# Kernel tuning notes

Measured on AMD Instinct MI355X. Metric: run time of the kernel, lower is better.

## Reference

```python
import jax, jax.numpy as jnp
import numpy as np

N_NODES = 100000
N_EDGES = 1600000
IN_DIM = 64
HID = 64
EDGE_DIM = 1
NUM_GRAPHS = 1000
SCALE = 0.05


def setup_inputs() -> dict:
    key = jax.random.key(0)
    ks = jax.random.split(key, 20)
    x = jax.random.normal(ks[0], (N_NODES, IN_DIM), dtype=jnp.float32)
    edge_index = jax.random.randint(ks[1], (2, N_EDGES), 0, N_NODES, dtype=jnp.int64)
    edge_attr = jax.random.normal(ks[2], (N_EDGES, EDGE_DIM), dtype=jnp.float32)
    batch = jnp.sort(jax.random.randint(ks[3], (N_NODES,), 0, NUM_GRAPHS, dtype=jnp.int64))
    p = lambda k, shp: SCALE * jax.random.normal(k, shp, dtype=jnp.float32)
    return {
        "x": x, "edge_index": edge_index, "edge_attr": edge_attr, "batch": batch,
        # conv1 MLP + edge lin
        "W1a": p(ks[4], (IN_DIM, HID)), "b1a": p(ks[5], (HID,)),
        "W1b": p(ks[6], (HID, HID)), "b1b": p(ks[7], (HID,)),
        "We1": p(ks[8], (EDGE_DIM, IN_DIM)), "be1": p(ks[9], (IN_DIM,)),
        # conv2 MLP + edge lin
        "W2a": p(ks[10], (HID, HID)), "b2a": p(ks[11], (HID,)),
        "W2b": p(ks[12], (HID, HID)), "b2b": p(ks[13], (HID,)),
        "We2": p(ks[14], (EDGE_DIM, HID)), "be2": p(ks[15], (HID,)),
        # classifier
        "Wc1": p(ks[16], (HID, HID)), "bc1": p(ks[17], (HID,)),
        "Wc2": p(ks[18], (HID, 1)), "bc2": p(ks[19], (1,)),
    }


def _gine(x, src, dst, e_proj, Wa, ba, Wb, bb):
    # message: ReLU(x_src + projected edge feature); scatter-sum to target
    msg = jax.nn.relu(x[src] + e_proj)                      # [E, D]
    agg = jax.ops.segment_sum(msg, dst, num_segments=x.shape[0])
    h = x + agg                                             # eps = 0 (default)
    return jax.nn.relu(h @ Wa + ba) @ Wb + bb               # GIN MLP


def reference(x, edge_index, edge_attr, batch,
              W1a, b1a, W1b, b1b, We1, be1,
              W2a, b2a, W2b, b2b, We2, be2,
              Wc1, bc1, Wc2, bc2):
    src, dst = edge_index[0], edge_index[1]
    h = _gine(x, src, dst, edge_attr @ We1 + be1, W1a, b1a, W1b, b1b)
    h = jax.nn.relu(h)  # dropout is identity in eval mode
    h = _gine(h, src, dst, edge_attr @ We2 + be2, W2a, b2a, W2b, b2b)
    h = jax.nn.relu(h)
    # global mean pool over graphs
    sums = jax.ops.segment_sum(h, batch, num_segments=NUM_GRAPHS)
    cnts = jax.ops.segment_sum(jnp.ones((h.shape[0], 1), h.dtype), batch, num_segments=NUM_GRAPHS)
    pooled = sums / jnp.maximum(cnts, 1.0)                  # [G, HID]
    return jax.nn.relu(pooled @ Wc1 + bc1) @ Wc2 + bc2      # [G, 1]
```

## Files before the change

### kernel.cpp

```cpp
#include <hip/hip_runtime.h>

#define N_NODES    100000
#define N_EDGES    1600000
#define DIM        64
#define NUM_GRAPHS 1000
#define CONV_BLK   3125
#define PAD        72

#define SLICES     512
#define SLICE_E    3125
#define NBUCK      782
#define CAP4       3072

typedef __attribute__((ext_vector_type(8))) short bf16x8;
typedef __attribute__((ext_vector_type(4))) float f32x4;

__device__ __forceinline__ unsigned short f2bf(float f) {
    unsigned int b = __float_as_uint(f);
    b += 0x7FFFu + ((b >> 16) & 1u);
    return (unsigned short)(b >> 16);
}

__device__ __forceinline__ float4 ntload_f4(const float* p) {
    f32x4 v = __builtin_nontemporal_load((const f32x4*)p);
    return make_float4(v.x, v.y, v.z, v.w);
}

__global__ __launch_bounds__(256) void prep(
    const int* __restrict__ ei, const float* __restrict__ x,
    int* __restrict__ hist, int* __restrict__ bucketTotal,
    unsigned short* __restrict__ x16)
{
    __shared__ int lh[NBUCK];
    int blk = blockIdx.x, t = threadIdx.x;
    if (blk < SLICES) {
        for (int i = t; i < NBUCK; i += 256) lh[i] = 0;
        __syncthreads();
        const int* dsts = ei + N_EDGES + blk * SLICE_E;
        for (int k = t; k < SLICE_E; k += 256)
            atomicAdd(&lh[dsts[k] >> 7], 1);
        __syncthreads();
        for (int i = t; i < NBUCK; i += 256) {
            int h = lh[i];
            hist[blk * NBUCK + i] = h;
            if (h) atomicAdd(&bucketTotal[i], h);
        }
    } else {
        int tt = (blk - SLICES) * 256 + t;
        if (tt < N_NODES * DIM / 8) {
            int base = tt * 8;
            float4 f0 = ntload_f4(x + base);
            float4 f1 = ntload_f4(x + base + 4);
            uint4 o;
            o.x = (unsigned)f2bf(f0.x) | ((unsigned)f2bf(f0.y) << 16);
            o.y = (unsigned)f2bf(f0.z) | ((unsigned)f2bf(f0.w) << 16);
            o.z = (unsigned)f2bf(f1.x) | ((unsigned)f2bf(f1.y) << 16);
            o.w = (unsigned)f2bf(f1.z) | ((unsigned)f2bf(f1.w) << 16);
            *(uint4*)(x16 + base) = o;
        }
    }
}

__global__ __launch_bounds__(1024) void csr_c2a(
    const int* __restrict__ bucketTotal, int* __restrict__ bucketStart)
{
    __shared__ int sc[1024];
    int t = threadIdx.x;
    int v = (t < NBUCK) ? bucketTotal[t] : 0;
    sc[t] = v;
    __syncthreads();
    for (int o = 1; o < 1024; o <<= 1) {
        int u = (t >= o) ? sc[t - o] : 0;
        __syncthreads();
        sc[t] += u;
        __syncthreads();
    }
    if (t < NBUCK) bucketStart[t] = sc[t] - v;
    if (t == NBUCK - 1) bucketStart[NBUCK] = sc[t];
}

__global__ __launch_bounds__(512) void csr_c2b(
    const int* __restrict__ hist, const int* __restrict__ bucketStart,
    int* __restrict__ off)
{
    __shared__ int sc[512];
    int b = blockIdx.x, t = threadIdx.x;
    int v = hist[t * NBUCK + b];
    sc[t] = v;
    __syncthreads();
    for (int o = 1; o < 512; o <<= 1) {
        int u = (t >= o) ? sc[t - o] : 0;
        __syncthreads();
        sc[t] += u;
        __syncthreads();
    }
    off[b * SLICES + t] = bucketStart[b] + sc[t] - v;
}

__global__ __launch_bounds__(256) void csr_c3(
    const int* __restrict__ ei, const float* __restrict__ ea,
    const int* __restrict__ hist, const int* __restrict__ off,
    int2* __restrict__ tmp)
{
    __shared__ int2 staging[SLICE_E];
    __shared__ int  lstart[NBUCK + 1];
    __shared__ int  garr[NBUCK];
    __shared__ int  lcur[NBUCK];
    __shared__ unsigned short barr[SLICE_E];
    __shared__ int  part[256];

    int s = blockIdx.x, t = threadIdx.x;

    int h[4];
    int mysum = 0;
    #pragma unroll
    for (int j = 0; j < 4; ++j) {
        int b = 4 * t + j;
        h[j] = (b < NBUCK) ? hist[s * NBUCK + b] : 0;
        mysum += h[j];
    }
    part[t] = mysum;
    for (int i = t; i < NBUCK; i += 256) {
        garr[i] = off[i * SLICES + s];
        lcur[i] = 0;
    }
    __syncthreads();
    for (int o = 1; o < 256; o <<= 1) {
        int u = (t >= o) ? part[t - o] : 0;
        __syncthreads();
        part[t] += u;
        __syncthreads();
    }
    int run = part[t] - mysum;
    #pragma unroll
    for (int j = 0; j < 4; ++j) {
        int b = 4 * t + j;
        if (b < NBUCK) lstart[b] = run;
        run += h[j];
    }
    if (t == 0) lstart[NBUCK] = SLICE_E;
    __syncthreads();

    #pragma unroll
    for (int j = 0; j < 4; ++j) {
        int b = 4 * t + j;
        if (b < NBUCK)
            for (int i = lstart[b]; i < lstart[b + 1]; ++i)
                barr[i] = (unsigned short)b;
    }
    __syncthreads();

    for (int k = t; k < SLICE_E; k += 256) {
        int e   = s * SLICE_E + k;
        int src = ei[e];
        int dst = ei[N_EDGES + e];
        float a = ea[e];
        int b   = dst >> 7;
        int p   = lstart[b] + atomicAdd(&lcur[b], 1);
        staging[p] = make_int2(((dst & 127) << 17) | src, __float_as_int(a));
    }
    __syncthreads();

    for (int i = t; i < SLICE_E; i += 256) {
        int b = barr[i];
        tmp[garr[b] + (i - lstart[b])] = staging[i];
    }
}

__global__ __launch_bounds__(256) void csr_c4(
    const int2* __restrict__ tmp, const int* __restrict__ bucketStart,
    int2* __restrict__ csr_e, int* __restrict__ rowptr)
{
    __shared__ int2 staging[CAP4];
    __shared__ int  nh[128];
    __shared__ int  nscan[128];
    __shared__ int  ncur[128];

    int b = blockIdx.x, t = threadIdx.x;
    int lo = bucketStart[b], hi = bucketStart[b + 1];
    int cnt = hi - lo;
    int node0 = b << 7;
    int nn = min(128, N_NODES - node0);

    if (t < 128) { nh[t] = 0; ncur[t] = 0; }
    __syncthreads();

    int2 r[12];
    int nr = 0;
    for (int k = t; k < cnt; k += 256) {
        int2 v = tmp[lo + k];
        r[nr++] = v;
        atomicAdd(&nh[v.x >> 17], 1);
    }
    __syncthreads();

    if (t < 128) nscan[t] = nh[t];
    __syncthreads();
    for (int o = 1; o < 128; o <<= 1) {
        int u = (t >= o && t < 128) ? nscan[t - o] : 0;
        __syncthreads();
        if (t < 128) nscan[t] += u;
        __syncthreads();
    }
    if (t < 128) nscan[t] -= nh[t];
    __syncthreads();

    if (t < nn) rowptr[node0 + t] = lo + nscan[t];
    if (b == NBUCK - 1 && t == 0) rowptr[N_NODES] = N_EDGES;

    for (int k = 0; k < nr; ++k) {
        int dl = r[k].x >> 17;
        int p  = nscan[dl] + atomicAdd(&ncur[dl], 1);
        staging[p] = r[k];
    }
    __syncthreads();

    for (int i = t; i < cnt; i += 256) {
        int2 v = staging[i];
        csr_e[lo + i] = make_int2((v.x & 0x1FFFF) << 4, v.y);
    }
}

template<bool SELF32>
__global__ __launch_bounds__(512, 8) void gine_mfma(
    const uint2* __restrict__ g2,
    const float* __restrict__ self32,
    const int*   __restrict__ rowptr,
    const int2*  __restrict__ csr_e,
    const float* __restrict__ We, const float* __restrict__ be,
    const float* __restrict__ Wa, const float* __restrict__ ba,
    const float* __restrict__ Wb, const float* __restrict__ bb,
    unsigned int* __restrict__ out16)
{
    __shared__ short sWat[64 * PAD];
    __shared__ short sWbt[64 * PAD];
    __shared__ short h16[32 * PAD];
    __shared__ short t16[32 * PAD];

    int t = threadIdx.x;
    for (int i = t; i < 4096; i += 512) {
        int k = i >> 6, n = i & 63;
        sWat[n * PAD + k] = (short)f2bf(Wa[i]);
        sWbt[n * PAD + k] = (short)f2bf(Wb[i]);
    }
    int wave = t >> 6;
    int lane = t & 63;
    int quad = lane >> 4;
    int l15  = lane & 15;
    int slot = wave * 4 + quad;
    int d0   = l15 * 4;
    float4 wp = *(const float4*)(We + d0);
    float4 bp = *(const float4*)(be + d0);
    int mtile = wave & 1;
    int ntile = wave >> 1;
    int col   = ntile * 16 + l15;
    int am    = mtile * 16 + l15;
    float bav = ba[col], bbv = bb[col];
    __syncthreads();

    for (int base = blockIdx.x * 32; base < N_NODES; base += gridDim.x * 32) {
        int  node  = base + slot;
        bool valid = node < N_NODES;
        int beg = 0, deg = 0;
        if (valid) { beg = rowptr[node]; deg = rowptr[node + 1] - beg; }
        int dm = deg;
        dm = max(dm, __shfl_xor(dm, 16));
        dm = max(dm, __shfl_xor(dm, 32));

        float4 agg = make_float4(0.f, 0.f, 0.f, 0.f);
        #define EDGE4(rr, uu, cond)                                              \
        {                                                                        \
            float s = (cond) ? 1.f : 0.f, av = __int_as_float(rr.y);             \
            float e0 = __uint_as_float(uu.x << 16);                              \
            float e1 = __uint_as_float(uu.x & 0xFFFF0000u);                      \
            float e2 = __uint_as_float(uu.y << 16);                              \
            float e3 = __uint_as_float(uu.y & 0xFFFF0000u);                      \
            agg.x = fmaf(s, fmaxf(e0 + fmaf(av, wp.x, bp.x), 0.f), agg.x);       \
            agg.y = fmaf(s, fmaxf(e1 + fmaf(av, wp.y, bp.y), 0.f), agg.y);       \
            agg.z = fmaf(s, fmaxf(e2 + fmaf(av, wp.z, bp.z), 0.f), agg.z);       \
            agg.w = fmaf(s, fmaxf(e3 + fmaf(av, wp.w, bp.w), 0.f), agg.w);       \
        }
        for (int j = 0; j < dm; j += 4) {
            int2 r0 = csr_e[beg + ((j + 0) < deg ? j + 0 : 0)];
            int2 r1 = csr_e[beg + ((j + 1) < deg ? j + 1 : 0)];
            int2 r2 = csr_e[beg + ((j + 2) < deg ? j + 2 : 0)];
            int2 r3 = csr_e[beg + ((j + 3) < deg ? j + 3 : 0)];
            uint2 u0 = g2[r0.x + l15];
            uint2 u1 = g2[r1.x + l15];
            uint2 u2 = g2[r2.x + l15];
            uint2 u3 = g2[r3.x + l15];
            EDGE4(r0, u0, (j + 0) < deg)
            EDGE4(r1, u1, (j + 1) < deg)
            EDGE4(r2, u2, (j + 2) < deg)
            EDGE4(r3, u3, (j + 3) < deg)
        }
        #undef EDGE4
        if (valid) {
            if (SELF32) {
                float4 sv = *(const float4*)(self32 + (size_t)node * DIM + d0);
                agg.x += sv.x; agg.y += sv.y; agg.z += sv.z; agg.w += sv.w;
            } else {
                uint2 u = g2[node * 16 + l15];
                agg.x += __uint_as_float(u.x << 16);
                agg.y += __uint_as_float(u.x & 0xFFFF0000u);
                agg.z += __uint_as_float(u.y << 16);
                agg.w += __uint_as_float(u.y & 0xFFFF0000u);
            }
        }
        {
            unsigned lo = (unsigned)f2bf(agg.x) | ((unsigned)f2bf(agg.y) << 16);
            unsigned hi = (unsigned)f2bf(agg.z) | ((unsigned)f2bf(agg.w) << 16);
            *(uint2*)&h16[slot * PAD + d0] = make_uint2(lo, hi);
        }
        __syncthreads();

        f32x4 acc = {bav, bav, bav, bav};
        #pragma unroll
        for (int s = 0; s < 2; ++s) {
            bf16x8 a = *(const bf16x8*)&h16[am * PAD + s * 32 + quad * 8];
            bf16x8 b = *(const bf16x8*)&sWat[col * PAD + s * 32 + quad * 8];
            acc = __builtin_amdgcn_mfma_f32_16x16x32_bf16(a, b, acc, 0, 0, 0);
        }
        #pragma unroll
        for (int r = 0; r < 4; ++r) {
            int row = mtile * 16 + quad * 4 + r;
            t16[row * PAD + col] = (short)f2bf(fmaxf(acc[r], 0.f));
        }
        __syncthreads();

        f32x4 acc2 = {bbv, bbv, bbv, bbv};
        #pragma unroll
        for (int s = 0; s < 2; ++s) {
            bf16x8 a = *(const bf16x8*)&t16[am * PAD + s * 32 + quad * 8];
            bf16x8 b = *(const bf16x8*)&sWbt[col * PAD + s * 32 + quad * 8];
            acc2 = __builtin_amdgcn_mfma_f32_16x16x32_bf16(a, b, acc2, 0, 0, 0);
        }
        #pragma unroll
        for (int r = 0; r < 4; ++r) {
            int row = mtile * 16 + quad * 4 + r;
            h16[row * PAD + col] = (short)f2bf(fmaxf(acc2[r], 0.f));
        }
        __syncthreads();
        {
            int nn = t >> 4, dd = (t & 15) * 2;
            if (base + nn < N_NODES) {
                uint2 v = *(const uint2*)&h16[nn * PAD + dd * 2];
                *(uint2*)&out16[(size_t)(base + nn) * 32 + dd] = v;
            }
        }
        __syncthreads();
    }
}

__device__ __forceinline__ int lbound(const int* __restrict__ a, int key) {
    int lo = 0, hi = N_NODES;
    while (lo < hi) {
        int mid = (lo + hi) >> 1;
        if (a[mid] < key) lo = mid + 1; else hi = mid;
    }
    return lo;
}

__global__ __launch_bounds__(256) void pool_cls(
    const unsigned int* __restrict__ B16b,
    const int* __restrict__ batch,
    const float* __restrict__ Wc1,  const float* __restrict__ bc1,
    const float* __restrict__ Wc2,  const float* __restrict__ bc2,
    float* __restrict__ out)
{
    __shared__ float sW[64 * 64];
    __shared__ float sp[4][64];

    int t = threadIdx.x;
    for (int i = t; i < 64 * 64; i += 256) sW[i] = Wc1[i];

    int nl   = t >> 6;
    int lane = t & 63;
    int g    = blockIdx.x * 4 + nl;

    int p = lane & 31, h = lane >> 5;
    if (g < NUM_GRAPHS) {
        int s = lbound(batch, g);
        int e = lbound(batch, g + 1);
        float2 sum = make_float2(0.f, 0.f);
        for (int i = s + h; i < e; i += 2) {
            unsigned u = B16b[(size_t)i * 32 + p];
            sum.x += __uint_as_float(u << 16);
            sum.y += __uint_as_float(u & 0xFFFF0000u);
        }
        sum.x += __shfl_xor(sum.x, 32);
        sum.y += __shfl_xor(sum.y, 32);
        if (h == 0) {
            float inv = 1.f / (float)max(e - s, 1);
            sp[nl][2 * p]     = sum.x * inv;
            sp[nl][2 * p + 1] = sum.y * inv;
        }
    } else if (h == 0) {
        sp[nl][2 * p] = 0.f;
        sp[nl][2 * p + 1] = 0.f;
    }
    __syncthreads();

    float acc = bc1[lane];
    #pragma unroll
    for (int k = 0; k < 64; ++k)
        acc = fmaf(sp[nl][k], sW[k * 64 + lane], acc);
    float tv = fmaxf(acc, 0.f) * Wc2[lane];

    #pragma unroll
    for (int off = 32; off > 0; off >>= 1)
        tv += __shfl_down(tv, off);

    if (lane == 0 && g < NUM_GRAPHS) out[g] = tv + bc2[0];
}

extern "C" void kernel_launch(void* const* d_in, const int* in_sizes, int n_in,
                              void* d_out, int out_size, void* d_ws, size_t ws_size,
                              hipStream_t stream) {
    const float* x     = (const float*)d_in[0];
    const int*   ei    = (const int*)  d_in[1];
    const float* ea    = (const float*)d_in[2];
    const int*   batch = (const int*)  d_in[3];
    const float* W1a = (const float*)d_in[4];
    const float* b1a = (const float*)d_in[5];
    const float* W1b = (const float*)d_in[6];
    const float* b1b = (const float*)d_in[7];
    const float* We1 = (const float*)d_in[8];
    const float* be1 = (const float*)d_in[9];
    const float* W2a = (const float*)d_in[10];
    const float* b2a = (const float*)d_in[11];
    const float* W2b = (const float*)d_in[12];
    const float* b2b = (const float*)d_in[13];
    const float* We2 = (const float*)d_in[14];
    const float* be2 = (const float*)d_in[15];
    const float* Wc1 = (const float*)d_in[16];
    const float* bc1 = (const float*)d_in[17];
    const float* Wc2 = (const float*)d_in[18];
    const float* bc2 = (const float*)d_in[19];

    int2*           csr_e  = (int2*)d_ws;
    unsigned short* x16    = (unsigned short*)(csr_e + N_EDGES);
    unsigned short* B16    = x16 + (size_t)N_NODES * DIM;
    unsigned short* B16b   = B16 + (size_t)N_NODES * DIM;
    int2*           tmp    = (int2*)B16b;
    int*            hist   = (int*)(B16b + (size_t)N_NODES * DIM);
    int*            off    = hist + SLICES * NBUCK;
    int*            bucketTotal = off + NBUCK * SLICES;
    int*            bucketStart = bucketTotal + NBUCK;
    int*            rowptr = bucketStart + (NBUCK + 1);

    hipMemsetAsync(bucketTotal, 0, NBUCK * sizeof(int), stream);

    prep<<<SLICES + CONV_BLK, 256, 0, stream>>>(ei, x, hist, bucketTotal, x16);
    csr_c2a<<<1, 1024, 0, stream>>>(bucketTotal, bucketStart);
    csr_c2b<<<NBUCK, 512, 0, stream>>>(hist, bucketStart, off);
    csr_c3<<<SLICES, 256, 0, stream>>>(ei, ea, hist, off, tmp);
    csr_c4<<<NBUCK, 256, 0, stream>>>(tmp, bucketStart, csr_e, rowptr);

    gine_mfma<true><<<1024, 512, 0, stream>>>(
        (const uint2*)x16, x, rowptr, csr_e,
        We1, be1, W1a, b1a, W1b, b1b, (unsigned int*)B16);

    gine_mfma<false><<<1024, 512, 0, stream>>>(
        (const uint2*)B16, nullptr, rowptr, csr_e,
        We2, be2, W2a, b2a, W2b, b2b, (unsigned int*)B16b);

    pool_cls<<<(NUM_GRAPHS + 3) / 4, 256, 0, stream>>>(
        (const unsigned int*)B16b, batch, Wc1, bc1, Wc2, bc2, (float*)d_out);
}
```

Measured before the change: 306.1 us.

## Degree-sort nodes per bucket and gather two edges per quad with 16-byte loads

csr_c4 now bitonic-sorts the 128 nodes of each bucket by in-degree and writes a permutation that packs degree and node id together. The gine kernels process nodes in that order, so the nodes sharing a wave have similar degree and less time is lost waiting on the wave's maximum degree. Each 16-lane group now splits into two halves that handle alternate edges with 8-channel uint4 gathers, then combines them with a shuffle. Outputs are scattered back to their original node rows. Launch bounds drop to 6 waves per SIMD to make room for the extra registers, and the perm buffer reuses the hist workspace.

```diff
diff --git a/kernel.cpp b/kernel.cpp
--- a/kernel.cpp
+++ b/kernel.cpp
@@ -169,12 +169,14 @@
 
 __global__ __launch_bounds__(256) void csr_c4(
     const int2* __restrict__ tmp, const int* __restrict__ bucketStart,
-    int2* __restrict__ csr_e, int* __restrict__ rowptr)
+    int2* __restrict__ csr_e, int* __restrict__ rowptr,
+    int* __restrict__ perm)
 {
     __shared__ int2 staging[CAP4];
     __shared__ int  nh[128];
     __shared__ int  nscan[128];
     __shared__ int  ncur[128];
+    __shared__ unsigned skey[128];
 
     int b = blockIdx.x, t = threadIdx.x;
     int lo = bucketStart[b], hi = bucketStart[b + 1];
@@ -217,15 +219,38 @@
 
     for (int i = t; i < cnt; i += 256) {
         int2 v = staging[i];
-        csr_e[lo + i] = make_int2((v.x & 0x1FFFF) << 4, v.y);
+        csr_e[lo + i] = make_int2((v.x & 0x1FFFF) << 3, v.y);
+    }
+
+    if (t < 128)
+        skey[t] = (t < nn) ? (((unsigned)nh[t] << 7) | (unsigned)t)
+                           : 0xFFFFFFFFu;
+    for (int k = 2; k <= 128; k <<= 1)
+        for (int jj = k >> 1; jj > 0; jj >>= 1) {
+            __syncthreads();
+            if (t < 128) {
+                int ixj = t ^ jj;
+                if (ixj > t) {
+                    unsigned a = skey[t], c = skey[ixj];
+                    bool asc = ((t & k) == 0);
+                    if ((a > c) == asc) { skey[t] = c; skey[ixj] = a; }
+                }
+            }
+        }
+    __syncthreads();
+    if (t < nn) {
+        unsigned e = skey[t];
+        int nd = node0 + (int)(e & 127u);
+        perm[node0 + t] = (int)(((e >> 7) << 17) | (unsigned)nd);
     }
 }
 
 template<bool SELF32>
-__global__ __launch_bounds__(512, 8) void gine_mfma(
+__global__ __launch_bounds__(512, 6) void gine_mfma(
     const uint2* __restrict__ g2,
     const float* __restrict__ self32,
     const int*   __restrict__ rowptr,
+    const int*   __restrict__ perm,
     const int2*  __restrict__ csr_e,
     const float* __restrict__ We, const float* __restrict__ be,
     const float* __restrict__ Wa, const float* __restrict__ ba,
@@ -247,70 +272,101 @@
     int lane = t & 63;
     int quad = lane >> 4;
     int l15  = lane & 15;
+    int half = l15 >> 3;
+    int l7   = lane & 7;
     int slot = wave * 4 + quad;
-    int d0   = l15 * 4;
-    float4 wp = *(const float4*)(We + d0);
-    float4 bp = *(const float4*)(be + d0);
+    int d0   = l7 * 8;
+    float4 w0 = *(const float4*)(We + d0);
+    float4 w1 = *(const float4*)(We + d0 + 4);
+    float4 bq0 = *(const float4*)(be + d0);
+    float4 bq1 = *(const float4*)(be + d0 + 4);
+    float wp[8] = {w0.x, w0.y, w0.z, w0.w, w1.x, w1.y, w1.z, w1.w};
+    float bp[8] = {bq0.x, bq0.y, bq0.z, bq0.w, bq1.x, bq1.y, bq1.z, bq1.w};
     int mtile = wave & 1;
     int ntile = wave >> 1;
     int col   = ntile * 16 + l15;
     int am    = mtile * 16 + l15;
     float bav = ba[col], bbv = bb[col];
+    const uint4* g4 = (const uint4*)g2;
     __syncthreads();
 
     for (int base = blockIdx.x * 32; base < N_NODES; base += gridDim.x * 32) {
-        int  node  = base + slot;
-        bool valid = node < N_NODES;
-        int beg = 0, deg = 0;
-        if (valid) { beg = rowptr[node]; deg = rowptr[node + 1] - beg; }
+        int  pslot = base + slot;
+        bool valid = pslot < N_NODES;
+        int  pe   = valid ? perm[pslot] : 0;
+        int  node = pe & 0x1FFFF;
+        int  deg  = (int)((unsigned)pe >> 17);
+        int  beg  = valid ? rowptr[node] : 0;
+        beg = min(beg, N_EDGES - 1);
         int dm = deg;
         dm = max(dm, __shfl_xor(dm, 16));
         dm = max(dm, __shfl_xor(dm, 32));
 
-        float4 agg = make_float4(0.f, 0.f, 0.f, 0.f);
-        #define EDGE4(rr, uu, cond)                                              \
+        float agg[8];
+        #pragma unroll
+        for (int k = 0; k < 8; ++k) agg[k] = 0.f;
+
+        #define EDGE8(rr, uu, cond)                                              \
         {                                                                        \
-            float s = (cond) ? 1.f : 0.f, av = __int_as_float(rr.y);             \
+            float s  = (cond) ? 1.f : 0.f;                                       \
+            float av = __int_as_float(rr.y);                                     \
             float e0 = __uint_as_float(uu.x << 16);                              \
             float e1 = __uint_as_float(uu.x & 0xFFFF0000u);                      \
             float e2 = __uint_as_float(uu.y << 16);                              \
             float e3 = __uint_as_float(uu.y & 0xFFFF0000u);                      \
-            agg.x = fmaf(s, fmaxf(e0 + fmaf(av, wp.x, bp.x), 0.f), agg.x);       \
-            agg.y = fmaf(s, fmaxf(e1 + fmaf(av, wp.y, bp.y), 0.f), agg.y);       \
-            agg.z = fmaf(s, fmaxf(e2 + fmaf(av, wp.z, bp.z), 0.f), agg.z);       \
-            agg.w = fmaf(s, fmaxf(e3 + fmaf(av, wp.w, bp.w), 0.f), agg.w);       \
-        }
+            float e4 = __uint_as_float(uu.z << 16);                              \
+            float e5 = __uint_as_float(uu.z & 0xFFFF0000u);                      \
+            float e6 = __uint_as_float(uu.w << 16);                              \
+            float e7 = __uint_as_float(uu.w & 0xFFFF0000u);                      \
+            agg[0] = fmaf(s, fmaxf(e0 + fmaf(av, wp[0], bp[0]), 0.f), agg[0]);   \
+            agg[1] = fmaf(s, fmaxf(e1 + fmaf(av, wp[1], bp[1]), 0.f), agg[1]);   \
+            agg[2] = fmaf(s, fmaxf(e2 + fmaf(av, wp[2], bp[2]), 0.f), agg[2]);   \
+            agg[3] = fmaf(s, fmaxf(e3 + fmaf(av, wp[3], bp[3]), 0.f), agg[3]);   \
+            agg[4] = fmaf(s, fmaxf(e4 + fmaf(av, wp[4], bp[4]), 0.f), agg[4]);   \
+            agg[5] = fmaf(s, fmaxf(e5 + fmaf(av, wp[5], bp[5]), 0.f), agg[5]);   \
+            agg[6] = fmaf(s, fmaxf(e6 + fmaf(av, wp[6], bp[6]), 0.f), agg[6]);   \
+            agg[7] = fmaf(s, fmaxf(e7 + fmaf(av, wp[7], bp[7]), 0.f), agg[7]);   \
+        }
+
         for (int j = 0; j < dm; j += 4) {
-            int2 r0 = csr_e[beg + ((j + 0) < deg ? j + 0 : 0)];
-            int2 r1 = csr_e[beg + ((j + 1) < deg ? j + 1 : 0)];
-            int2 r2 = csr_e[beg + ((j + 2) < deg ? j + 2 : 0)];
-            int2 r3 = csr_e[beg + ((j + 3) < deg ? j + 3 : 0)];
-            uint2 u0 = g2[r0.x + l15];
-            uint2 u1 = g2[r1.x + l15];
-            uint2 u2 = g2[r2.x + l15];
-            uint2 u3 = g2[r3.x + l15];
-            EDGE4(r0, u0, (j + 0) < deg)
-            EDGE4(r1, u1, (j + 1) < deg)
-            EDGE4(r2, u2, (j + 2) < deg)
-            EDGE4(r3, u3, (j + 3) < deg)
-        }
-        #undef EDGE4
-        if (valid) {
-            if (SELF32) {
-                float4 sv = *(const float4*)(self32 + (size_t)node * DIM + d0);
-                agg.x += sv.x; agg.y += sv.y; agg.z += sv.z; agg.w += sv.w;
-            } else {
-                uint2 u = g2[node * 16 + l15];
-                agg.x += __uint_as_float(u.x << 16);
-                agg.y += __uint_as_float(u.x & 0xFFFF0000u);
-                agg.z += __uint_as_float(u.y << 16);
-                agg.w += __uint_as_float(u.y & 0xFFFF0000u);
+            int j0 = j + half, j1 = j + 2 + half;
+            int2 ra = csr_e[beg + (j0 < deg ? j0 : 0)];
+            int2 rb = csr_e[beg + (j1 < deg ? j1 : 0)];
+            uint4 ua = g4[ra.x + l7];
+            uint4 ub = g4[rb.x + l7];
+            EDGE8(ra, ua, j0 < deg)
+            EDGE8(rb, ub, j1 < deg)
+        }
+        #undef EDGE8
+
+        #pragma unroll
+        for (int k = 0; k < 8; ++k) agg[k] += __shfl_xor(agg[k], 8);
+
+        if (half == 0) {
+            if (valid) {
+                if (SELF32) {
+                    float4 s0 = *(const float4*)(self32 + (size_t)node * DIM + d0);
+                    float4 s1 = *(const float4*)(self32 + (size_t)node * DIM + d0 + 4);
+                    agg[0] += s0.x; agg[1] += s0.y; agg[2] += s0.z; agg[3] += s0.w;
+                    agg[4] += s1.x; agg[5] += s1.y; agg[6] += s1.z; agg[7] += s1.w;
+                } else {
+                    uint4 u = g4[node * 8 + l7];
+                    agg[0] += __uint_as_float(u.x << 16);
+                    agg[1] += __uint_as_float(u.x & 0xFFFF0000u);
+                    agg[2] += __uint_as_float(u.y << 16);
+                    agg[3] += __uint_as_float(u.y & 0xFFFF0000u);
+                    agg[4] += __uint_as_float(u.z << 16);
+                    agg[5] += __uint_as_float(u.z & 0xFFFF0000u);
+                    agg[6] += __uint_as_float(u.w << 16);
+                    agg[7] += __uint_as_float(u.w & 0xFFFF0000u);
+                }
             }
-        }
-        {
-            unsigned lo = (unsigned)f2bf(agg.x) | ((unsigned)f2bf(agg.y) << 16);
-            unsigned hi = (unsigned)f2bf(agg.z) | ((unsigned)f2bf(agg.w) << 16);
-            *(uint2*)&h16[slot * PAD + d0] = make_uint2(lo, hi);
+            uint4 o;
+            o.x = (unsigned)f2bf(agg[0]) | ((unsigned)f2bf(agg[1]) << 16);
+            o.y = (unsigned)f2bf(agg[2]) | ((unsigned)f2bf(agg[3]) << 16);
+            o.z = (unsigned)f2bf(agg[4]) | ((unsigned)f2bf(agg[5]) << 16);
+            o.w = (unsigned)f2bf(agg[6]) | ((unsigned)f2bf(agg[7]) << 16);
+            *(uint4*)&h16[slot * PAD + d0] = o;
         }
         __syncthreads();
 
@@ -343,9 +399,11 @@
         __syncthreads();
         {
             int nn = t >> 4, dd = (t & 15) * 2;
-            if (base + nn < N_NODES) {
+            int ps = base + nn;
+            if (ps < N_NODES) {
+                int nd = perm[ps] & 0x1FFFF;
                 uint2 v = *(const uint2*)&h16[nn * PAD + dd * 2];
-                *(uint2*)&out16[(size_t)(base + nn) * 32 + dd] = v;
+                *(uint2*)&out16[(size_t)nd * 32 + dd] = v;
             }
         }
         __syncthreads();
@@ -448,6 +506,7 @@
     int*            bucketTotal = off + NBUCK * SLICES;
     int*            bucketStart = bucketTotal + NBUCK;
     int*            rowptr = bucketStart + (NBUCK + 1);
+    int*            perm   = hist;
 
     hipMemsetAsync(bucketTotal, 0, NBUCK * sizeof(int), stream);
 
@@ -455,14 +514,14 @@
     csr_c2a<<<1, 1024, 0, stream>>>(bucketTotal, bucketStart);
     csr_c2b<<<NBUCK, 512, 0, stream>>>(hist, bucketStart, off);
     csr_c3<<<SLICES, 256, 0, stream>>>(ei, ea, hist, off, tmp);
-    csr_c4<<<NBUCK, 256, 0, stream>>>(tmp, bucketStart, csr_e, rowptr);
+    csr_c4<<<NBUCK, 256, 0, stream>>>(tmp, bucketStart, csr_e, rowptr, perm);
 
     gine_mfma<true><<<1024, 512, 0, stream>>>(
-        (const uint2*)x16, x, rowptr, csr_e,
+        (const uint2*)x16, x, rowptr, perm, csr_e,
         We1, be1, W1a, b1a, W1b, b1b, (unsigned int*)B16);
 
     gine_mfma<false><<<1024, 512, 0, stream>>>(
-        (const uint2*)B16, nullptr, rowptr, csr_e,
+        (const uint2*)B16, nullptr, rowptr, perm, csr_e,
         We2, be2, W2a, b2a, W2b, b2b, (unsigned int*)B16b);
 
     pool_cls<<<(NUM_GRAPHS + 3) / 4, 256, 0, stream>>>(
```

After: 328.7 us. +7.4%, slower.

## Sort nodes by degree within 128-node chunks to balance wave edge loops

Applied to the files above, without the earlier changes.

Adds a bitonic-sort kernel that orders each 128-node chunk by in-degree and packs degree with node id into a permutation array. The GINE kernels now process nodes in permuted order, so the 16 nodes sharing a wave have similar degrees and the per-wave max-degree loop wastes fewer masked iterations. Output rows are scattered back through the permutation. The cost is an extra kernel launch, an extra perm load per node, and less contiguous output writes and neighbor locality.

```diff
diff --git a/kernel.cpp b/kernel.cpp
--- a/kernel.cpp
+++ b/kernel.cpp
@@ -221,11 +221,44 @@
     }
 }
 
+__global__ __launch_bounds__(128) void build_perm(
+    const int* __restrict__ rowptr, int* __restrict__ perm)
+{
+    __shared__ unsigned skey[128];
+    int b = blockIdx.x, t = threadIdx.x;
+    int node0 = b << 7;
+    int nn = min(128, N_NODES - node0);
+
+    unsigned key = 0xFFFFFFFFu;
+    if (t < nn) {
+        int d = rowptr[node0 + t + 1] - rowptr[node0 + t];
+        key = ((unsigned)d << 7) | (unsigned)t;
+    }
+    skey[t] = key;
+    for (int k = 2; k <= 128; k <<= 1)
+        for (int j = k >> 1; j > 0; j >>= 1) {
+            __syncthreads();
+            int ixj = t ^ j;
+            if (ixj > t) {
+                unsigned a = skey[t], c = skey[ixj];
+                bool asc = ((t & k) == 0);
+                if ((a > c) == asc) { skey[t] = c; skey[ixj] = a; }
+            }
+        }
+    __syncthreads();
+    if (t < nn) {
+        unsigned e = skey[t];
+        int nd = node0 + (int)(e & 127u);
+        perm[node0 + t] = (int)(((e >> 7) << 17) | (unsigned)nd);
+    }
+}
+
 template<bool SELF32>
 __global__ __launch_bounds__(512, 8) void gine_mfma(
     const uint2* __restrict__ g2,
     const float* __restrict__ self32,
     const int*   __restrict__ rowptr,
+    const int*   __restrict__ perm,
     const int2*  __restrict__ csr_e,
     const float* __restrict__ We, const float* __restrict__ be,
     const float* __restrict__ Wa, const float* __restrict__ ba,
@@ -259,10 +292,13 @@
     __syncthreads();
 
     for (int base = blockIdx.x * 32; base < N_NODES; base += gridDim.x * 32) {
-        int  node  = base + slot;
-        bool valid = node < N_NODES;
-        int beg = 0, deg = 0;
-        if (valid) { beg = rowptr[node]; deg = rowptr[node + 1] - beg; }
+        int  pslot = base + slot;
+        bool valid = pslot < N_NODES;
+        int  pe   = valid ? perm[pslot] : 0;
+        int  node = pe & 0x1FFFF;
+        int  deg  = (int)((unsigned)pe >> 17);
+        int  beg  = 0;
+        if (valid) beg = min(rowptr[node], N_EDGES - 1);
         int dm = deg;
         dm = max(dm, __shfl_xor(dm, 16));
         dm = max(dm, __shfl_xor(dm, 32));
@@ -343,9 +379,11 @@
         __syncthreads();
         {
             int nn = t >> 4, dd = (t & 15) * 2;
-            if (base + nn < N_NODES) {
+            int ps = base + nn;
+            if (ps < N_NODES) {
+                int nd = perm[ps] & 0x1FFFF;
                 uint2 v = *(const uint2*)&h16[nn * PAD + dd * 2];
-                *(uint2*)&out16[(size_t)(base + nn) * 32 + dd] = v;
+                *(uint2*)&out16[(size_t)nd * 32 + dd] = v;
             }
         }
         __syncthreads();
@@ -448,6 +486,7 @@
     int*            bucketTotal = off + NBUCK * SLICES;
     int*            bucketStart = bucketTotal + NBUCK;
     int*            rowptr = bucketStart + (NBUCK + 1);
+    int*            perm   = hist;
 
     hipMemsetAsync(bucketTotal, 0, NBUCK * sizeof(int), stream);
 
@@ -456,13 +495,14 @@
     csr_c2b<<<NBUCK, 512, 0, stream>>>(hist, bucketStart, off);
     csr_c3<<<SLICES, 256, 0, stream>>>(ei, ea, hist, off, tmp);
     csr_c4<<<NBUCK, 256, 0, stream>>>(tmp, bucketStart, csr_e, rowptr);
+    build_perm<<<NBUCK, 128, 0, stream>>>(rowptr, perm);
 
     gine_mfma<true><<<1024, 512, 0, stream>>>(
-        (const uint2*)x16, x, rowptr, csr_e,
+        (const uint2*)x16, x, rowptr, perm, csr_e,
         We1, be1, W1a, b1a, W1b, b1b, (unsigned int*)B16);
 
     gine_mfma<false><<<1024, 512, 0, stream>>>(
-        (const uint2*)B16, nullptr, rowptr, csr_e,
+        (const uint2*)B16, nullptr, rowptr, perm, csr_e,
         We2, be2, W2a, b2a, W2b, b2b, (unsigned int*)B16b);
 
     pool_cls<<<(NUM_GRAPHS + 3) / 4, 256, 0, stream>>>(
```

Result: no change. 308.6 us (+0.8%).
